# Performance work log

Measured on AMD Instinct MI355X. Metric: run time of the kernel, lower is better.

The kernel has to match this reference:

```python
import jax, jax.numpy as jnp
import numpy as np

B, N, D = 4, 2048, 512   # batch, seq, feed_forward_size
H, DK, DV = 8, 64, 64    # heads, key_dim, value_dim
LN_EPS = 1e-5


def setup_inputs() -> dict:
    key = jax.random.key(0)
    ks = jax.random.split(key, 12)
    s = 0.02
    x = jax.random.normal(ks[0], (B, N, D), dtype=jnp.float32)
    # boolean mask, True = masked out (torch masked_fill semantics); causal
    attn_mask = ~jnp.tril(jnp.ones((N, N), dtype=bool))[None, None]
    ln_g = jnp.ones((D,), jnp.float32)
    ln_b = jnp.zeros((D,), jnp.float32)
    wq = jax.random.normal(ks[1], (D, H * DK), jnp.float32) * s
    bq = jnp.zeros((H * DK,), jnp.float32)
    wk = jax.random.normal(ks[2], (D, H * DK), jnp.float32) * s
    bk = jnp.zeros((H * DK,), jnp.float32)
    wv = jax.random.normal(ks[3], (D, H * DV), jnp.float32) * s
    bv = jnp.zeros((H * DV,), jnp.float32)
    wo = jax.random.normal(ks[4], (H * DV, D), jnp.float32) * s
    bo = jnp.zeros((D,), jnp.float32)
    return {"x": x, "attn_mask": attn_mask, "ln_g": ln_g, "ln_b": ln_b,
            "wq": wq, "bq": bq, "wk": wk, "bk": bk, "wv": wv, "bv": bv,
            "wo": wo, "bo": bo}


def _layernorm(x, g, b):
    mu = jnp.mean(x, axis=-1, keepdims=True)
    var = jnp.mean(jnp.square(x - mu), axis=-1, keepdims=True)
    return (x - mu) * jax.lax.rsqrt(var + LN_EPS) * g + b


def reference(x, attn_mask, ln_g, ln_b, wq, bq, wk, bk, wv, bv, wo, bo):
    xn = _layernorm(x, ln_g, ln_b)
    scale = DK ** -0.5
    q = (xn @ wq + bq).reshape(B, N, H, DK).transpose(0, 2, 1, 3) * scale  # b h n d
    k = (xn @ wk + bk).reshape(B, N, H, DK).transpose(0, 2, 1, 3)
    v = (xn @ wv + bv).reshape(B, N, H, DV).transpose(0, 2, 1, 3)
    sim = jnp.einsum('bhid,bhjd->bhij', q, k)
    sim = jnp.where(attn_mask, -jnp.finfo(sim.dtype).max, sim)
    attn = jax.nn.softmax(sim, axis=-1)  # dropout p=0 (eval)
    out = jnp.einsum('bhij,bhjd->bhid', attn, v)
    out = out.transpose(0, 2, 1, 3).reshape(B, N, H * DV)  # b n (h d)
    return out @ wo + bo
```

## Files before the change

### kernel.cpp

```cpp
#include <hip/hip_runtime.h>

typedef unsigned short u16;
typedef unsigned long long u64;
typedef __bf16 bf16x8 __attribute__((ext_vector_type(8)));
typedef float f32x4 __attribute__((ext_vector_type(4)));
typedef float f32x16 __attribute__((ext_vector_type(16)));

#define H_HEADS 8
#define DHEAD 64
#define NSEQ 2048
#define DMODEL 512
#define BATCH 4
#define MROWS (BATCH * NSEQ)
#define BH (BATCH * H_HEADS)

__device__ __forceinline__ u16 f2bf(float f) {
  unsigned u = __builtin_bit_cast(unsigned, f);
  u += 0x7fffu + ((u >> 16) & 1u);
  return (u16)(u >> 16);
}

__device__ __forceinline__ bf16x8 ldfrag(const u16* p) {
  return __builtin_bit_cast(bf16x8, *(const uint4*)p);
}

typedef __attribute__((address_space(1))) void GV;
typedef __attribute__((address_space(3))) void LV;
__device__ __forceinline__ void gld16(const void* g, void* l) {
  __builtin_amdgcn_global_load_lds((GV*)g, (LV*)l, 16, 0, 0);
}

__global__ __launch_bounds__(256) void ln_kernel(
    const float* __restrict__ x, const float* __restrict__ g,
    const float* __restrict__ b, u16* __restrict__ xn) {
  const int row = blockIdx.x;
  const int t = threadIdx.x;
  const float2 v = *(const float2*)(x + (size_t)row * DMODEL + t * 2);
  float s = v.x + v.y;
  float ss = v.x * v.x + v.y * v.y;
  #pragma unroll
  for (int d = 1; d < 64; d <<= 1) {
    s += __shfl_xor(s, d);
    ss += __shfl_xor(ss, d);
  }
  __shared__ float red[8];
  const int wave = t >> 6, lane = t & 63;
  if (lane == 0) { red[wave] = s; red[4 + wave] = ss; }
  __syncthreads();
  s = red[0] + red[1] + red[2] + red[3];
  ss = red[4] + red[5] + red[6] + red[7];
  const float mean = s * (1.0f / DMODEL);
  const float var = ss * (1.0f / DMODEL) - mean * mean;
  const float rstd = rsqrtf(var + 1e-5f);
  const float2 gg = *(const float2*)(g + t * 2);
  const float2 bb = *(const float2*)(b + t * 2);
  const float o0 = (v.x - mean) * rstd * gg.x + bb.x;
  const float o1 = (v.y - mean) * rstd * gg.y + bb.y;
  const unsigned packed = (unsigned)f2bf(o0) | ((unsigned)f2bf(o1) << 16);
  *(unsigned*)(xn + (size_t)row * DMODEL + t * 2) = packed;
}

__global__ __launch_bounds__(256) void transpose_w4_kernel(
    const float* __restrict__ w0, const float* __restrict__ w1,
    const float* __restrict__ w2, const float* __restrict__ w3,
    u16* __restrict__ WT) {
  __shared__ float tile[32][33];
  const int z = blockIdx.z;
  const float* W = (z == 0) ? w0 : (z == 1) ? w1 : (z == 2) ? w2 : w3;
  u16* dst = WT + (size_t)z * DMODEL * DMODEL;
  const int n0 = blockIdx.x * 32, k0 = blockIdx.y * 32;
  const int t = threadIdx.x;
  #pragma unroll
  for (int p = 0; p < 4; ++p) {
    const int u = p * 256 + t;
    const int r = u >> 5, c = u & 31;
    tile[r][c] = W[(size_t)(k0 + r) * DMODEL + n0 + c];
  }
  __syncthreads();
  #pragma unroll
  for (int p = 0; p < 4; ++p) {
    const int u = p * 256 + t;
    const int rn = u >> 5, ck = u & 31;
    dst[(size_t)(n0 + rn) * DMODEL + k0 + ck] = f2bf(tile[ck][rn]);
  }
}

template <int MODE>
__global__ __launch_bounds__(256) void gemm128_kernel(
    const u16* __restrict__ A, const u16* __restrict__ BT,
    const float* __restrict__ bq, const float* __restrict__ bk,
    const float* __restrict__ bv,
    u16* __restrict__ qb, u16* __restrict__ kb, u16* __restrict__ vtb,
    float* __restrict__ fout, int K) {
  __shared__ u16 lds_a[128 * 64];
  __shared__ u16 lds_b[128 * 64];
  const int t = threadIdx.x;
  const int lane = t & 63, wave = t >> 6;
  const int wm = wave >> 1, wn = wave & 1;
  const int lo = lane & 15, hi = lane >> 4;
  const int m0 = blockIdx.y * 128, n0 = blockIdx.x * 128;
  const int sr = lane >> 3;
  const int scol = (((lane & 7) ^ sr) * 8);
  f32x4 acc[4][4] = {};
  for (int k0 = 0; k0 < K; k0 += 64) {
    #pragma unroll
    for (int j = 0; j < 4; ++j) {
      const int ch = wave * 4 + j;
      gld16(A + (size_t)(m0 + ch * 8 + sr) * K + k0 + scol, lds_a + ch * 512);
      gld16(BT + (size_t)(n0 + ch * 8 + sr) * K + k0 + scol, lds_b + ch * 512);
    }
    __syncthreads();
    #pragma unroll
    for (int kc = 0; kc < 2; ++kc) {
      bf16x8 af[4], bfr[4];
      const int sw = ((lo & 7) * 8);
      #pragma unroll
      for (int i = 0; i < 4; ++i)
        af[i] = ldfrag(lds_a + (wm * 64 + i * 16 + lo) * 64 + ((kc * 32 + hi * 8) ^ sw));
      #pragma unroll
      for (int i = 0; i < 4; ++i)
        bfr[i] = ldfrag(lds_b + (wn * 64 + i * 16 + lo) * 64 + ((kc * 32 + hi * 8) ^ sw));
      __builtin_amdgcn_s_setprio(1);
      #pragma unroll
      for (int mi = 0; mi < 4; ++mi)
        #pragma unroll
        for (int ni = 0; ni < 4; ++ni)
          acc[mi][ni] = __builtin_amdgcn_mfma_f32_16x16x32_bf16(
              af[mi], bfr[ni], acc[mi][ni], 0, 0, 0);
      __builtin_amdgcn_s_setprio(0);
    }
    __syncthreads();
  }
  #pragma unroll
  for (int mi = 0; mi < 4; ++mi) {
    #pragma unroll
    for (int ni = 0; ni < 4; ++ni) {
      const int col = n0 + wn * 64 + ni * 16 + lo;
      if (MODE == 0) {
        const int mat = col >> 9, w = col & 511;
        const int hh = w >> 6, dk = w & 63;
        const float bi = (mat == 0 ? bq : (mat == 1 ? bk : bv))[w];
        const int row0 = m0 + wm * 64 + mi * 16 + hi * 4;
        const int bbx = row0 >> 11, seq0 = row0 & 2047;
        if (mat == 2) {
          u64 pk = 0;
          #pragma unroll
          for (int r = 0; r < 4; ++r)
            pk |= (u64)f2bf(acc[mi][ni][r] + bi) << (16 * r);
          *(u64*)(vtb + ((size_t)(bbx * H_HEADS + hh) * DHEAD + dk) * NSEQ + seq0) = pk;
        } else {
          const float sc = (mat == 0) ? 0.18033688f : 1.0f;
          u16* dst = (mat == 0 ? qb : kb);
          #pragma unroll
          for (int r = 0; r < 4; ++r)
            dst[(((size_t)(bbx * H_HEADS + hh) * NSEQ) + seq0 + r) * DHEAD + dk] =
                f2bf((acc[mi][ni][r] + bi) * sc);
        }
      } else {
        const float bi = bq[col];
        #pragma unroll
        for (int r = 0; r < 4; ++r) {
          const int row = m0 + wm * 64 + mi * 16 + hi * 4 + r;
          fout[(size_t)row * DMODEL + col] = acc[mi][ni][r] + bi;
        }
      }
    }
  }
}

__global__ __launch_bounds__(256, 4) void attn_kernel(
    const u16* __restrict__ Q, const u16* __restrict__ K,
    const u16* __restrict__ VT, u16* __restrict__ O,
    float* __restrict__ pO, float* __restrict__ pML) {
  __shared__ u16 lds_k[2][4096];
  __shared__ u16 lds_v[2][4096];
  const int t = threadIdx.x;
  const int lane = t & 63, wave = t >> 6;
  const int l31 = lane & 31, hi = lane >> 5;
  const int l7 = lane & 7;

  const int n = blockIdx.x;
  const int bh = n / 40;
  const int r = n % 40;
  int qt, ck, C;
  if (r < 4)       { qt = r;                 C = 1; ck = 0; }
  else if (r < 12) { qt = 4 + ((r - 4) >> 1);  C = 2; ck = (r - 4) & 1; }
  else if (r < 24) { qt = 8 + (r - 12) / 3;    C = 3; ck = (r - 12) % 3; }
  else             { qt = 12 + ((r - 24) >> 2); C = 4; ck = (r - 24) & 3; }
  const int T = 2 * qt + 2;
  const int kc0 = ck * 8;
  const int L = min(8, T - kc0);

  const int b = bh >> 3, h = bh & 7;
  const u16* Qh = Q + (size_t)bh * NSEQ * DHEAD;
  const u16* Kh = K + (size_t)bh * NSEQ * DHEAD;
  const u16* Vh = VT + (size_t)bh * DHEAD * NSEQ;

  const int q0w = qt * 128 + wave * 32;
  const int lastkt = (q0w + 31) >> 6;
  const int qrow = q0w + l31;

  bf16x8 qf[4];
  #pragma unroll
  for (int c = 0; c < 4; ++c)
    qf[c] = ldfrag(Qh + (size_t)qrow * DHEAD + c * 16 + hi * 8);

  f32x16 o0 = {}, o1 = {};
  float m = -INFINITY, l = 0.0f;

  const int sr = lane >> 3;
  const int scol = ((lane & 7) ^ sr) * 8;
  const int swz = l7 * 8;

  #pragma unroll
  for (int j = 0; j < 2; ++j) {
    const int ch = wave * 2 + j;
    gld16(Kh + (size_t)(kc0 * 64 + ch * 8 + sr) * DHEAD + scol, lds_k[0] + ch * 512);
    gld16(Vh + (size_t)(ch * 8 + sr) * NSEQ + kc0 * 64 + scol, lds_v[0] + ch * 512);
  }

  for (int lt = 0; lt < L; ++lt) {
    const int gk = kc0 + lt;
    const int cur = lt & 1;
    if (lt + 1 < L) {
      const int kvn = (gk + 1) * 64;
      #pragma unroll
      for (int j = 0; j < 2; ++j) {
        const int ch = wave * 2 + j;
        gld16(Kh + (size_t)(kvn + ch * 8 + sr) * DHEAD + scol, lds_k[cur ^ 1] + ch * 512);
        gld16(Vh + (size_t)(ch * 8 + sr) * NSEQ + kvn + scol, lds_v[cur ^ 1] + ch * 512);
      }
      asm volatile("s_waitcnt vmcnt(4)" ::: "memory");
    } else {
      asm volatile("s_waitcnt vmcnt(0)" ::: "memory");
    }
    __builtin_amdgcn_s_barrier();
    __builtin_amdgcn_sched_barrier(0);

    if (gk <= lastkt) {
      const u16* lk = lds_k[cur];
      const u16* lv = lds_v[cur];
      f32x16 st0 = {}, st1 = {};

      __builtin_amdgcn_s_setprio(1);
      #pragma unroll
      for (int c = 0; c < 4; ++c) {
        const int col = (c * 16 + hi * 8) ^ swz;
        bf16x8 kf0 = ldfrag(lk + l31 * 64 + col);
        bf16x8 kf1 = ldfrag(lk + (32 + l31) * 64 + col);
        st0 = __builtin_amdgcn_mfma_f32_32x32x16_bf16(kf0, qf[c], st0, 0, 0, 0);
        st1 = __builtin_amdgcn_mfma_f32_32x32x16_bf16(kf1, qf[c], st1, 0, 0, 0);
      }
      __builtin_amdgcn_s_setprio(0);

      if (gk == lastkt) {
        const int kvb = gk * 64 + 4 * hi;
        #pragma unroll
        for (int rr = 0; rr < 16; ++rr) {
          const int kv = kvb + (rr & 3) + 8 * (rr >> 2);
          if (kv > qrow) st0[rr] = -1e30f;
          if (kv + 32 > qrow) st1[rr] = -1e30f;
        }
      }

      float pm = st0[0];
      #pragma unroll
      for (int rr = 1; rr < 16; ++rr) pm = fmaxf(pm, st0[rr]);
      #pragma unroll
      for (int rr = 0; rr < 16; ++rr) pm = fmaxf(pm, st1[rr]);
      pm = fmaxf(pm, __shfl_xor(pm, 32));
      const float mn = fmaxf(m, pm);
      const float sc = exp2f(m - mn);
      m = mn;
      float ps = 0.0f;
      #pragma unroll
      for (int rr = 0; rr < 16; ++rr) { st0[rr] = exp2f(st0[rr] - mn); ps += st0[rr]; }
      #pragma unroll
      for (int rr = 0; rr < 16; ++rr) { st1[rr] = exp2f(st1[rr] - mn); ps += st1[rr]; }
      ps += __shfl_xor(ps, 32);
      l = l * sc + ps;
      #pragma unroll
      for (int rr = 0; rr < 16; ++rr) { o0[rr] *= sc; o1[rr] *= sc; }

      bf16x8 pf0, pf1, pf2, pf3;
      {
        unsigned w0, w1, w2, w3, w4, w5, w6, w7;
        asm("v_cvt_pk_bf16_f32 %0, %1, %2" : "=v"(w0) : "v"(st0[0]), "v"(st0[1]));
        asm("v_cvt_pk_bf16_f32 %0, %1, %2" : "=v"(w1) : "v"(st0[2]), "v"(st0[3]));
        asm("v_cvt_pk_bf16_f32 %0, %1, %2" : "=v"(w2) : "v"(st0[4]), "v"(st0[5]));
        asm("v_cvt_pk_bf16_f32 %0, %1, %2" : "=v"(w3) : "v"(st0[6]), "v"(st0[7]));
        asm("v_cvt_pk_bf16_f32 %0, %1, %2" : "=v"(w4) : "v"(st0[8]), "v"(st0[9]));
        asm("v_cvt_pk_bf16_f32 %0, %1, %2" : "=v"(w5) : "v"(st0[10]), "v"(st0[11]));
        asm("v_cvt_pk_bf16_f32 %0, %1, %2" : "=v"(w6) : "v"(st0[12]), "v"(st0[13]));
        asm("v_cvt_pk_bf16_f32 %0, %1, %2" : "=v"(w7) : "v"(st0[14]), "v"(st0[15]));
        asm("v_permlane32_swap_b32 %0, %1" : "+v"(w0), "+v"(w2));
        asm("v_permlane32_swap_b32 %0, %1" : "+v"(w1), "+v"(w3));
        asm("v_permlane32_swap_b32 %0, %1" : "+v"(w4), "+v"(w6));
        asm("v_permlane32_swap_b32 %0, %1" : "+v"(w5), "+v"(w7));
        union Uu { unsigned u[4]; bf16x8 v; };
        Uu a; a.u[0] = w0; a.u[1] = w1; a.u[2] = w2; a.u[3] = w3; pf0 = a.v;
        Uu bb; bb.u[0] = w4; bb.u[1] = w5; bb.u[2] = w6; bb.u[3] = w7; pf1 = bb.v;
      }
      {
        unsigned w0, w1, w2, w3, w4, w5, w6, w7;
        asm("v_cvt_pk_bf16_f32 %0, %1, %2" : "=v"(w0) : "v"(st1[0]), "v"(st1[1]));
        asm("v_cvt_pk_bf16_f32 %0, %1, %2" : "=v"(w1) : "v"(st1[2]), "v"(st1[3]));
        asm("v_cvt_pk_bf16_f32 %0, %1, %2" : "=v"(w2) : "v"(st1[4]), "v"(st1[5]));
        asm("v_cvt_pk_bf16_f32 %0, %1, %2" : "=v"(w3) : "v"(st1[6]), "v"(st1[7]));
        asm("v_cvt_pk_bf16_f32 %0, %1, %2" : "=v"(w4) : "v"(st1[8]), "v"(st1[9]));
        asm("v_cvt_pk_bf16_f32 %0, %1, %2" : "=v"(w5) : "v"(st1[10]), "v"(st1[11]));
        asm("v_cvt_pk_bf16_f32 %0, %1, %2" : "=v"(w6) : "v"(st1[12]), "v"(st1[13]));
        asm("v_cvt_pk_bf16_f32 %0, %1, %2" : "=v"(w7) : "v"(st1[14]), "v"(st1[15]));
        asm("v_permlane32_swap_b32 %0, %1" : "+v"(w0), "+v"(w2));
        asm("v_permlane32_swap_b32 %0, %1" : "+v"(w1), "+v"(w3));
        asm("v_permlane32_swap_b32 %0, %1" : "+v"(w4), "+v"(w6));
        asm("v_permlane32_swap_b32 %0, %1" : "+v"(w5), "+v"(w7));
        union Uu { unsigned u[4]; bf16x8 v; };
        Uu a; a.u[0] = w0; a.u[1] = w1; a.u[2] = w2; a.u[3] = w3; pf2 = a.v;
        Uu bb; bb.u[0] = w4; bb.u[1] = w5; bb.u[2] = w6; bb.u[3] = w7; pf3 = bb.v;
      }

      __builtin_amdgcn_s_setprio(1);
      #pragma unroll
      for (int c = 0; c < 4; ++c) {
        const int col = (c * 16 + hi * 8) ^ swz;
        bf16x8 vf0 = ldfrag(lv + l31 * 64 + col);
        bf16x8 vf1 = ldfrag(lv + (32 + l31) * 64 + col);
        const bf16x8 pc = (c == 0) ? pf0 : (c == 1) ? pf1 : (c == 2) ? pf2 : pf3;
        o0 = __builtin_amdgcn_mfma_f32_32x32x16_bf16(vf0, pc, o0, 0, 0, 0);
        o1 = __builtin_amdgcn_mfma_f32_32x32x16_bf16(vf1, pc, o1, 0, 0, 0);
      }
      __builtin_amdgcn_s_setprio(0);
    }
    __builtin_amdgcn_sched_barrier(0);
    __builtin_amdgcn_s_barrier();
    __builtin_amdgcn_sched_barrier(0);
  }

  if (C == 1) {
    const float rl = __builtin_amdgcn_rcpf(l);
    u16* Ob = O + ((size_t)b * NSEQ + qrow) * DMODEL + h * DHEAD;
    #pragma unroll
    for (int d = 0; d < 2; ++d) {
      #pragma unroll
      for (int mq = 0; mq < 4; ++mq) {
        u64 pk = 0;
        #pragma unroll
        for (int c3 = 0; c3 < 4; ++c3) {
          const float v = (d ? o1[mq * 4 + c3] : o0[mq * 4 + c3]) * rl;
          pk |= (u64)f2bf(v) << (16 * c3);
        }
        *(u64*)(Ob + d * 32 + mq * 8 + hi * 4) = pk;
      }
    }
  } else {
    const int rloc = wave * 32 + l31;
    float* po = pO + (size_t)n * (128 * 64) + (size_t)rloc * 64;
    #pragma unroll
    for (int mq = 0; mq < 4; ++mq) {
      f32x4 v0 = {o0[mq * 4], o0[mq * 4 + 1], o0[mq * 4 + 2], o0[mq * 4 + 3]};
      *(f32x4*)(po + mq * 8 + hi * 4) = v0;
      f32x4 v1 = {o1[mq * 4], o1[mq * 4 + 1], o1[mq * 4 + 2], o1[mq * 4 + 3]};
      *(f32x4*)(po + 32 + mq * 8 + hi * 4) = v1;
    }
    if (hi == 0) {
      pML[(size_t)n * 256 + rloc] = m;
      pML[(size_t)n * 256 + 128 + rloc] = l;
    }
  }
}

__global__ __launch_bounds__(256) void attn_merge_kernel(
    const float* __restrict__ pO, const float* __restrict__ pML,
    u16* __restrict__ O) {
  const int u = blockIdx.x;
  const int bh = u / 12, qi = u % 12;
  const int qt = 4 + qi;
  const int C = (qt >> 2) + 1;
  int off;
  if (qt < 8) off = 4 + 2 * (qt - 4);
  else if (qt < 12) off = 12 + 3 * (qt - 8);
  else off = 24 + 4 * (qt - 12);
  const int slot0 = bh * 40 + off;
  const int t = threadIdx.x;
  const int row = t >> 1, db = (t & 1) * 32;

  float mc[4], lc[4];
  #pragma unroll
  for (int c = 0; c < 4; ++c) {
    if (c < C) {
      mc[c] = pML[(size_t)(slot0 + c) * 256 + row];
      lc[c] = pML[(size_t)(slot0 + c) * 256 + 128 + row];
    } else { mc[c] = -INFINITY; lc[c] = 0.0f; }
  }
  float ms = fmaxf(fmaxf(mc[0], mc[1]), fmaxf(mc[2], mc[3]));
  float w[4], ls = 0.0f;
  #pragma unroll
  for (int c = 0; c < 4; ++c) {
    w[c] = (c < C) ? exp2f(mc[c] - ms) : 0.0f;
    ls += w[c] * lc[c];
  }
  const float rl = __builtin_amdgcn_rcpf(ls);

  f32x4 a[8] = {};
  #pragma unroll
  for (int c = 0; c < 4; ++c) {
    if (c < C) {
      const float* src = pO + (size_t)(slot0 + c) * (128 * 64) + (size_t)row * 64 + db;
      const float wc = w[c];
      #pragma unroll
      for (int k = 0; k < 8; ++k) {
        const f32x4 v = *(const f32x4*)(src + k * 4);
        a[k] += v * wc;
      }
    }
  }
  const int b = bh >> 3, h = bh & 7;
  u16* dst = O + ((size_t)b * NSEQ + qt * 128 + row) * DMODEL + h * DHEAD + db;
  #pragma unroll
  for (int k = 0; k < 8; k += 1) {
    u64 pk = 0;
    #pragma unroll
    for (int j = 0; j < 4; ++j)
      pk |= (u64)f2bf(a[k][j] * rl) << (16 * j);
    *(u64*)(dst + k * 4) = pk;
  }
}

extern "C" void kernel_launch(void* const* d_in, const int* in_sizes, int n_in,
                              void* d_out, int out_size, void* d_ws, size_t ws_size,
                              hipStream_t stream) {
  const float* x = (const float*)d_in[0];
  const float* ln_g = (const float*)d_in[2];
  const float* ln_b = (const float*)d_in[3];
  const float* wq = (const float*)d_in[4];
  const float* bq = (const float*)d_in[5];
  const float* wk = (const float*)d_in[6];
  const float* bk = (const float*)d_in[7];
  const float* wv = (const float*)d_in[8];
  const float* bv = (const float*)d_in[9];
  const float* wo = (const float*)d_in[10];
  const float* bo = (const float*)d_in[11];

  char* ws = (char*)d_ws;
  u16* xn = (u16*)ws;     ws += (size_t)MROWS * DMODEL * 2;
  u16* wqkvT = (u16*)ws;  ws += (size_t)4 * DMODEL * DMODEL * 2;
  u16* woT = wqkvT + (size_t)3 * DMODEL * DMODEL;
  u16* qb = (u16*)ws;     ws += (size_t)MROWS * DMODEL * 2;
  u16* kb = (u16*)ws;     ws += (size_t)MROWS * DMODEL * 2;
  u16* vtb = (u16*)ws;    ws += (size_t)MROWS * DMODEL * 2;
  u16* attnb = (u16*)ws;  ws += (size_t)MROWS * DMODEL * 2;
  float* pO = (float*)ws; ws += (size_t)1280 * 128 * 64 * 4;
  float* pML = (float*)ws; ws += (size_t)1280 * 256 * 4;

  ln_kernel<<<MROWS, 256, 0, stream>>>(x, ln_g, ln_b, xn);
  transpose_w4_kernel<<<dim3(16, 16, 4), 256, 0, stream>>>(wq, wk, wv, wo, wqkvT);

  gemm128_kernel<0><<<dim3(12, 64), 256, 0, stream>>>(
      xn, wqkvT, bq, bk, bv, qb, kb, vtb, nullptr, DMODEL);

  attn_kernel<<<1280, 256, 0, stream>>>(qb, kb, vtb, attnb, pO, pML);
  attn_merge_kernel<<<384, 256, 0, stream>>>(pO, pML, attnb);

  gemm128_kernel<1><<<dim3(4, 64), 256, 0, stream>>>(
      attnb, woT, bo, nullptr, nullptr, nullptr, nullptr, nullptr,
      (float*)d_out, DMODEL);
}
```

Measured before the change: 112.4 us.

## Widen GEMM to 8 waves, swizzle block order, lazy softmax rescale in attention

The GEMM kernel now runs 512 threads (8 waves laid out 2x4), so each wave computes a 64x32 sub-tile instead of 64x64, and block IDs are remapped so consecutive blocks spread across XCD-style groups of 8. The attention kernel remaps its block index the same way, stride by 8. Its online softmax now takes tree-reduced max and sum and only rescales the accumulators when the new max exceeds the running max by more than 8 (log2 domain). This removes most per-tile rescale multiplies and shortens reduction dependency chains, at the cost of fp32 values up to 2^8 before normalization and halved per-wave GEMM work.

Result: faster. 108.4 us (-3.5%).

```diff
diff --git a/kernel.cpp b/kernel.cpp
--- a/kernel.cpp
+++ b/kernel.cpp
@@ -86,7 +86,7 @@
 }
 
 template <int MODE>
-__global__ __launch_bounds__(256) void gemm128_kernel(
+__global__ __launch_bounds__(512) void gemm128_kernel(
     const u16* __restrict__ A, const u16* __restrict__ BT,
     const float* __restrict__ bq, const float* __restrict__ bk,
     const float* __restrict__ bv,
@@ -96,35 +96,38 @@
   __shared__ u16 lds_b[128 * 64];
   const int t = threadIdx.x;
   const int lane = t & 63, wave = t >> 6;
-  const int wm = wave >> 1, wn = wave & 1;
+  const int wm = wave >> 2, wn = wave & 3;
   const int lo = lane & 15, hi = lane >> 4;
-  const int m0 = blockIdx.y * 128, n0 = blockIdx.x * 128;
+  const int nwg = gridDim.x * gridDim.y;
+  const int lid = blockIdx.y * gridDim.x + blockIdx.x;
+  const int sid = (lid & 7) * (nwg >> 3) + (lid >> 3);
+  const int m0 = (sid / gridDim.x) * 128, n0 = (sid % gridDim.x) * 128;
   const int sr = lane >> 3;
   const int scol = (((lane & 7) ^ sr) * 8);
-  f32x4 acc[4][4] = {};
+  f32x4 acc[4][2] = {};
   for (int k0 = 0; k0 < K; k0 += 64) {
     #pragma unroll
-    for (int j = 0; j < 4; ++j) {
-      const int ch = wave * 4 + j;
+    for (int j = 0; j < 2; ++j) {
+      const int ch = wave * 2 + j;
       gld16(A + (size_t)(m0 + ch * 8 + sr) * K + k0 + scol, lds_a + ch * 512);
       gld16(BT + (size_t)(n0 + ch * 8 + sr) * K + k0 + scol, lds_b + ch * 512);
     }
     __syncthreads();
     #pragma unroll
     for (int kc = 0; kc < 2; ++kc) {
-      bf16x8 af[4], bfr[4];
+      bf16x8 af[4], bfr[2];
       const int sw = ((lo & 7) * 8);
       #pragma unroll
       for (int i = 0; i < 4; ++i)
         af[i] = ldfrag(lds_a + (wm * 64 + i * 16 + lo) * 64 + ((kc * 32 + hi * 8) ^ sw));
       #pragma unroll
-      for (int i = 0; i < 4; ++i)
-        bfr[i] = ldfrag(lds_b + (wn * 64 + i * 16 + lo) * 64 + ((kc * 32 + hi * 8) ^ sw));
+      for (int i = 0; i < 2; ++i)
+        bfr[i] = ldfrag(lds_b + (wn * 32 + i * 16 + lo) * 64 + ((kc * 32 + hi * 8) ^ sw));
       __builtin_amdgcn_s_setprio(1);
       #pragma unroll
       for (int mi = 0; mi < 4; ++mi)
         #pragma unroll
-        for (int ni = 0; ni < 4; ++ni)
+        for (int ni = 0; ni < 2; ++ni)
           acc[mi][ni] = __builtin_amdgcn_mfma_f32_16x16x32_bf16(
               af[mi], bfr[ni], acc[mi][ni], 0, 0, 0);
       __builtin_amdgcn_s_setprio(0);
@@ -134,8 +137,8 @@
   #pragma unroll
   for (int mi = 0; mi < 4; ++mi) {
     #pragma unroll
-    for (int ni = 0; ni < 4; ++ni) {
-      const int col = n0 + wn * 64 + ni * 16 + lo;
+    for (int ni = 0; ni < 2; ++ni) {
+      const int col = n0 + wn * 32 + ni * 16 + lo;
       if (MODE == 0) {
         const int mat = col >> 9, w = col & 511;
         const int hh = w >> 6, dk = w & 63;
@@ -179,7 +182,8 @@
   const int l31 = lane & 31, hi = lane >> 5;
   const int l7 = lane & 7;
 
-  const int n = blockIdx.x;
+  const int nraw = blockIdx.x;
+  const int n = (nraw & 7) * 160 + (nraw >> 3);
   const int bh = n / 40;
   const int r = n % 40;
   int qt, ck, C;
@@ -263,24 +267,36 @@
         }
       }
 
-      float pm = st0[0];
-      #pragma unroll
-      for (int rr = 1; rr < 16; ++rr) pm = fmaxf(pm, st0[rr]);
-      #pragma unroll
-      for (int rr = 0; rr < 16; ++rr) pm = fmaxf(pm, st1[rr]);
-      pm = fmaxf(pm, __shfl_xor(pm, 32));
-      const float mn = fmaxf(m, pm);
-      const float sc = exp2f(m - mn);
-      m = mn;
-      float ps = 0.0f;
-      #pragma unroll
-      for (int rr = 0; rr < 16; ++rr) { st0[rr] = exp2f(st0[rr] - mn); ps += st0[rr]; }
-      #pragma unroll
-      for (int rr = 0; rr < 16; ++rr) { st1[rr] = exp2f(st1[rr] - mn); ps += st1[rr]; }
-      ps += __shfl_xor(ps, 32);
-      l = l * sc + ps;
-      #pragma unroll
-      for (int rr = 0; rr < 16; ++rr) { o0[rr] *= sc; o1[rr] *= sc; }
+      float mx[16];
+      #pragma unroll
+      for (int i = 0; i < 16; ++i) mx[i] = fmaxf(st0[i], st1[i]);
+      #pragma unroll
+      for (int stp = 8; stp; stp >>= 1)
+        #pragma unroll
+        for (int i = 0; i < stp; ++i) mx[i] = fmaxf(mx[i], mx[i + stp]);
+      float pm = fmaxf(mx[0], __shfl_xor(mx[0], 32));
+
+      if (__any(pm > m + 8.0f)) {
+        const float mn = fmaxf(m, pm);
+        const float sc = exp2f(m - mn);
+        m = mn;
+        l *= sc;
+        #pragma unroll
+        for (int rr = 0; rr < 16; ++rr) { o0[rr] *= sc; o1[rr] *= sc; }
+      }
+
+      #pragma unroll
+      for (int rr = 0; rr < 16; ++rr) st0[rr] = exp2f(st0[rr] - m);
+      #pragma unroll
+      for (int rr = 0; rr < 16; ++rr) st1[rr] = exp2f(st1[rr] - m);
+      float sm[16];
+      #pragma unroll
+      for (int i = 0; i < 16; ++i) sm[i] = st0[i] + st1[i];
+      #pragma unroll
+      for (int stp = 8; stp; stp >>= 1)
+        #pragma unroll
+        for (int i = 0; i < stp; ++i) sm[i] += sm[i + stp];
+      l += sm[0] + __shfl_xor(sm[0], 32);
 
       bf16x8 pf0, pf1, pf2, pf3;
       {
@@ -456,13 +472,13 @@
   ln_kernel<<<MROWS, 256, 0, stream>>>(x, ln_g, ln_b, xn);
   transpose_w4_kernel<<<dim3(16, 16, 4), 256, 0, stream>>>(wq, wk, wv, wo, wqkvT);
 
-  gemm128_kernel<0><<<dim3(12, 64), 256, 0, stream>>>(
+  gemm128_kernel<0><<<dim3(12, 64), 512, 0, stream>>>(
       xn, wqkvT, bq, bk, bv, qb, kb, vtb, nullptr, DMODEL);
 
   attn_kernel<<<1280, 256, 0, stream>>>(qb, kb, vtb, attnb, pO, pML);
   attn_merge_kernel<<<384, 256, 0, stream>>>(pO, pML, attnb);
 
-  gemm128_kernel<1><<<dim3(4, 64), 256, 0, stream>>>(
+  gemm128_kernel<1><<<dim3(4, 64), 512, 0, stream>>>(
       attnb, woT, bo, nullptr, nullptr, nullptr, nullptr, nullptr,
       (float*)d_out, DMODEL);
 }
```
